# Kernel optimization log

Measured on AMD Instinct MI355X. Metric: run time of the kernel, lower is better.

The kernel has to match this reference:

```python
import jax, jax.numpy as jnp
import numpy as np

N_NODES = 100000
N_EDGES = 3200000
IN_CH = 256
OUT_CH = 10


def setup_inputs() -> dict:
    key = jax.random.key(0)
    k1, k2, k3, k4 = jax.random.split(key, 4)
    x = jax.random.normal(k1, (N_NODES, IN_CH), dtype=jnp.float32)
    edge_index = jax.random.randint(k2, (2, N_EDGES), 0, N_NODES, dtype=jnp.int64)
    W_mu = jax.random.normal(k3, (IN_CH, OUT_CH), dtype=jnp.float32) * (1.0 / np.sqrt(IN_CH))
    b_mu = jnp.zeros((OUT_CH,), dtype=jnp.float32)
    W_logstd = jax.random.normal(k4, (IN_CH, OUT_CH), dtype=jnp.float32) * (1.0 / np.sqrt(IN_CH))
    b_logstd = jnp.zeros((OUT_CH,), dtype=jnp.float32)
    return {"x": x, "edge_index": edge_index, "W_mu": W_mu, "b_mu": b_mu,
            "W_logstd": W_logstd, "b_logstd": b_logstd}


def _gcn_norm(edge_index, num_nodes):
    # PyG gcn_norm: add self loops, deg from target (col), norm = d^-1/2[row]*d^-1/2[col]
    loop = jnp.arange(num_nodes, dtype=edge_index.dtype)
    row = jnp.concatenate([edge_index[0], loop])  # source nodes
    col = jnp.concatenate([edge_index[1], loop])  # target nodes
    deg = jax.ops.segment_sum(jnp.ones_like(col, dtype=jnp.float32), col,
                              num_segments=num_nodes)
    dinv = jax.lax.rsqrt(jnp.maximum(deg, 1.0))  # self loops guarantee deg>=1
    norm = dinv[row] * dinv[col]  # [E+N]
    return row, col, norm


def _gcn_conv(x, W, b, row, col, norm, num_nodes):
    h = x @ W                               # [N, out]  linear transform first
    msg = h[row] * norm[:, None]            # gather + scale, [E+N, out]
    out = jax.ops.segment_sum(msg, col, num_segments=num_nodes)  # scatter-add
    return out + b


def reference(x, edge_index, W_mu, b_mu, W_logstd, b_logstd):
    n = x.shape[0]
    row, col, norm = _gcn_norm(edge_index, n)
    mu = _gcn_conv(x, W_mu, b_mu, row, col, norm, n)
    logstd = _gcn_conv(x, W_logstd, b_logstd, row, col, norm, n)
    return mu, logstd
```

## Files before the change

### kernel.cpp

```cpp
#include <hip/hip_runtime.h>
#include <math.h>

#define N_NODES 100000
#define N_EDGES 3200000
#define IN_CH 256
#define NC 20
#define OC 10
#define NPB 128
#define NBUCK 782
#define CAP 4864

#define CHUNK3 8192
#define NCHUNK3 391

__global__ __launch_bounds__(256) void k_initptr(int* __restrict__ bptr) {
    int i = blockIdx.x * 256 + threadIdx.x;
    if (i < NBUCK) bptr[i] = i * CAP;
}

__global__ __launch_bounds__(1024) void k_bin3(const int* __restrict__ row,
                                               const int* __restrict__ col,
                                               int* __restrict__ bptr,
                                               int* __restrict__ bpairs) {
    __shared__ int   lh[NBUCK];
    __shared__ int   lscan[NBUCK];
    __shared__ int   gmino[NBUCK];
    __shared__ int   stage[CHUNK3];
    __shared__ unsigned short sbkt[CHUNK3];

    int t = threadIdx.x;
    int e0 = blockIdx.x * CHUNK3;
    int nE = N_EDGES - e0; if (nE > CHUNK3) nE = CHUNK3;
    int n4 = nE >> 2;
    const int4* c4 = (const int4*)(col + e0);
    const int4* r4 = (const int4*)(row + e0);

    for (int i = t; i < NBUCK; i += 1024) lh[i] = 0;
    __syncthreads();

    for (int j = t; j < n4; j += 1024) {
        int4 c = c4[j];
        atomicAdd(&lh[c.x >> 7], 1); atomicAdd(&lh[c.y >> 7], 1);
        atomicAdd(&lh[c.z >> 7], 1); atomicAdd(&lh[c.w >> 7], 1);
    }
    __syncthreads();

    int cnt = 0;
    if (t < NBUCK) { cnt = lh[t]; lscan[t] = cnt; }
    __syncthreads();
    for (int o = 1; o < NBUCK; o <<= 1) {
        int add = 0;
        if (t < NBUCK && t >= o) add = lscan[t - o];
        __syncthreads();
        if (t < NBUCK) lscan[t] += add;
        __syncthreads();
    }
    if (t < NBUCK) {
        int lofs = lscan[t] - cnt;
        int gbase = cnt ? atomicAdd(&bptr[t], cnt) : 0;
        gmino[t] = gbase - lofs;
        lh[t] = lofs;
    }
    __syncthreads();

    for (int j = t; j < n4; j += 1024) {
        int4 c = c4[j];
        int4 r = r4[j];
        int b0 = c.x >> 7, b1 = c.y >> 7, b2 = c.z >> 7, b3 = c.w >> 7;
        int s0 = atomicAdd(&lh[b0], 1);
        int s1 = atomicAdd(&lh[b1], 1);
        int s2 = atomicAdd(&lh[b2], 1);
        int s3 = atomicAdd(&lh[b3], 1);
        stage[s0] = (r.x << 7) | (c.x & 127); sbkt[s0] = (unsigned short)b0;
        stage[s1] = (r.y << 7) | (c.y & 127); sbkt[s1] = (unsigned short)b1;
        stage[s2] = (r.z << 7) | (c.z & 127); sbkt[s2] = (unsigned short)b2;
        stage[s3] = (r.w << 7) | (c.w & 127); sbkt[s3] = (unsigned short)b3;
    }
    __syncthreads();

    for (int j = t; j < nE; j += 1024) {
        int b = sbkt[j];
        int dst = gmino[b] + j;
        if (dst < (b + 1) * CAP) bpairs[dst] = stage[j];
    }
}

__global__ __launch_bounds__(256) void k_deg(const int* __restrict__ bptr,
                                             const int* __restrict__ bpairs,
                                             float* __restrict__ dinv) {
    __shared__ int lc[NPB];
    int b = blockIdx.x, t = threadIdx.x;
    if (t < NPB) lc[t] = 0;
    __syncthreads();
    int start = b * CAP;
    int n = bptr[b] - start; if (n > CAP) n = CAP;
    for (int p = t; p < n; p += 256)
        atomicAdd(&lc[bpairs[start + p] & 127], 1);
    __syncthreads();
    int node = b * NPB + t;
    if (t < NPB && node < N_NODES)
        dinv[node] = rsqrtf((float)(lc[t] + 1));
}

__device__ __forceinline__ unsigned bfpack(float a, float b) {
    unsigned ua = __float_as_uint(a), ub = __float_as_uint(b);
    ua = (ua + 0x7FFFu + ((ua >> 16) & 1u)) >> 16;
    ub = (ub + 0x7FFFu + ((ub >> 16) & 1u)) >> 16;
    return ua | (ub << 16);
}
__device__ __forceinline__ float bflo(unsigned p) { return __uint_as_float(p << 16); }
__device__ __forceinline__ float bfhi(unsigned p) { return __uint_as_float(p & 0xFFFF0000u); }

__global__ __launch_bounds__(256) void k_gemm6(const float* __restrict__ x,
                                               const float* __restrict__ Wmu,
                                               const float* __restrict__ Wls,
                                               const float* __restrict__ dinv,
                                               unsigned* __restrict__ hbf) {
    __shared__ float sW[NC * 272];
    int t = threadIdx.x;
    for (int idx = t; idx < IN_CH * OC; idx += 256) {
        int k = idx / OC, c = idx - (idx / OC) * OC;
        int kk = k >> 6, j = k & 63;
        sW[c * 272 + kk * 68 + j]          = Wmu[idx];
        sW[(c + OC) * 272 + kk * 68 + j]   = Wls[idx];
    }
    __syncthreads();

    int kk = t & 3;
    int slot = t >> 2;
    int n0 = blockIdx.x * 128 + slot;

    int nd[2];
#pragma unroll
    for (int u = 0; u < 2; u++) {
        int n = n0 + u * 64;
        nd[u] = (n < N_NODES) ? n : (N_NODES - 1);
    }

    float acc[2][NC];
#pragma unroll
    for (int u = 0; u < 2; u++)
#pragma unroll
        for (int c = 0; c < NC; c++) acc[u][c] = 0.0f;

    const float4* x4 = (const float4*)x;

#pragma unroll 4
    for (int j4 = 0; j4 < 16; j4++) {
        float4 xv0 = x4[(size_t)nd[0] * 64 + kk * 16 + j4];
        float4 xv1 = x4[(size_t)nd[1] * 64 + kk * 16 + j4];
#pragma unroll
        for (int c = 0; c < NC; c++) {
            float4 w = *(const float4*)&sW[c * 272 + kk * 68 + j4 * 4];
            acc[0][c] += xv0.x * w.x + xv0.y * w.y + xv0.z * w.z + xv0.w * w.w;
            acc[1][c] += xv1.x * w.x + xv1.y * w.y + xv1.z * w.z + xv1.w * w.w;
        }
    }

#pragma unroll
    for (int u = 0; u < 2; u++)
#pragma unroll
        for (int c = 0; c < NC; c++) {
            acc[u][c] += __shfl_xor(acc[u][c], 2);
            acc[u][c] += __shfl_xor(acc[u][c], 1);
        }

    if (kk == 0) {
#pragma unroll
        for (int u = 0; u < 2; u++) {
            int n = n0 + u * 64;
            if (n >= N_NODES) continue;
            float d = dinv[n];
            unsigned* hp = hbf + (size_t)n * 10;
            *(uint2*)(hp + 0) = make_uint2(bfpack(acc[u][0] * d,  acc[u][1] * d),
                                           bfpack(acc[u][2] * d,  acc[u][3] * d));
            *(uint2*)(hp + 2) = make_uint2(bfpack(acc[u][4] * d,  acc[u][5] * d),
                                           bfpack(acc[u][6] * d,  acc[u][7] * d));
            *(uint2*)(hp + 4) = make_uint2(bfpack(acc[u][8] * d,  acc[u][9] * d),
                                           bfpack(acc[u][10] * d, acc[u][11] * d));
            *(uint2*)(hp + 6) = make_uint2(bfpack(acc[u][12] * d, acc[u][13] * d),
                                           bfpack(acc[u][14] * d, acc[u][15] * d));
            *(uint2*)(hp + 8) = make_uint2(bfpack(acc[u][16] * d, acc[u][17] * d),
                                           bfpack(acc[u][18] * d, acc[u][19] * d));
        }
    }
}

__global__ __launch_bounds__(256) void k_agg4(const int* __restrict__ bptr,
                                              const int* __restrict__ bpairs,
                                              const unsigned* __restrict__ hbf,
                                              const float* __restrict__ bmu,
                                              const float* __restrict__ bls,
                                              float* __restrict__ out) {
    __shared__ int lcnt[NPB];
    __shared__ int lscan[NPB];
    __shared__ int sCnt[NPB];
    __shared__ int ssrc[CAP];
    int b = blockIdx.x, t = threadIdx.x;
    int start = b * CAP;
    int n = bptr[b] - start; if (n > CAP) n = CAP;

    if (t < NPB) lcnt[t] = 0;
    __syncthreads();
    for (int p = t; p < n; p += 256)
        atomicAdd(&lcnt[bpairs[start + p] & 127], 1);
    __syncthreads();

    int cnt = 0;
    if (t < NPB) { cnt = lcnt[t]; lscan[t] = cnt; sCnt[t] = cnt; }
    __syncthreads();
    for (int o = 1; o < NPB; o <<= 1) {
        int add = 0;
        if (t < NPB && t >= o) add = lscan[t - o];
        __syncthreads();
        if (t < NPB) lscan[t] += add;
        __syncthreads();
    }
    if (t < NPB) lcnt[t] = lscan[t] - cnt;
    __syncthreads();

    for (int p = t; p < n; p += 256) {
        int pk = bpairs[start + p];
        int q = atomicAdd(&lcnt[pk & 127], 1);
        ssrc[q] = ((unsigned)pk) >> 7;
    }
    __syncthreads();

    int nl = t >> 1, half = t & 1;
    int node = b * NPB + nl;
    int ccnt = sCnt[nl];
    int base = lscan[nl] - ccnt;
    int mid = ccnt >> 1;
    int j0 = half ? mid : 0;
    int j1 = half ? ccnt : mid;

    float a[NC];
#pragma unroll
    for (int c = 0; c < NC; c++) a[c] = 0.0f;

#define ADDROW(R)                                                        \
    {                                                                    \
        const unsigned* hp_ = hbf + (size_t)(R) * 10;                    \
        uint2 q0 = *(const uint2*)(hp_ + 0);                             \
        uint2 q1 = *(const uint2*)(hp_ + 2);                             \
        uint2 q2 = *(const uint2*)(hp_ + 4);                             \
        uint2 q3 = *(const uint2*)(hp_ + 6);                             \
        uint2 q4 = *(const uint2*)(hp_ + 8);                             \
        a[0]  += bflo(q0.x); a[1]  += bfhi(q0.x);                        \
        a[2]  += bflo(q0.y); a[3]  += bfhi(q0.y);                        \
        a[4]  += bflo(q1.x); a[5]  += bfhi(q1.x);                        \
        a[6]  += bflo(q1.y); a[7]  += bfhi(q1.y);                        \
        a[8]  += bflo(q2.x); a[9]  += bfhi(q2.x);                        \
        a[10] += bflo(q2.y); a[11] += bfhi(q2.y);                        \
        a[12] += bflo(q3.x); a[13] += bfhi(q3.x);                        \
        a[14] += bflo(q3.y); a[15] += bfhi(q3.y);                        \
        a[16] += bflo(q4.x); a[17] += bfhi(q4.x);                        \
        a[18] += bflo(q4.y); a[19] += bfhi(q4.y);                        \
    }

    int j = j0;
    for (; j + 1 < j1; j += 2) {
        int r0 = ssrc[base + j];
        int r1 = ssrc[base + j + 1];
        ADDROW(r0);
        ADDROW(r1);
    }
    if (j < j1) {
        int r0 = ssrc[base + j];
        ADDROW(r0);
    }
    if (half == 0 && node < N_NODES) ADDROW(node);
#undef ADDROW

#pragma unroll
    for (int c = 0; c < NC; c++) a[c] += __shfl_xor(a[c], 1);

    if (half == 0 && node < N_NODES) {
        float dn = rsqrtf((float)(ccnt + 1));
        float* om = out + (size_t)node * OC;
        float* ol = out + (size_t)N_NODES * OC + (size_t)node * OC;
#pragma unroll
        for (int c = 0; c < OC; c++) {
            om[c] = dn * a[c]      + bmu[c];
            ol[c] = dn * a[c + OC] + bls[c];
        }
    }
}

__global__ __launch_bounds__(256) void k_init_deg(float* __restrict__ deg) {
    int i = blockIdx.x * 256 + threadIdx.x;
    if (i < N_NODES) deg[i] = 1.0f;
}
__global__ __launch_bounds__(256) void k_count(const int* __restrict__ col, float* __restrict__ deg) {
    int e = blockIdx.x * 256 + threadIdx.x;
    if (e < N_EDGES) atomicAdd(&deg[col[e]], 1.0f);
}
__global__ __launch_bounds__(256) void k_dinvk(float* __restrict__ deg) {
    int i = blockIdx.x * 256 + threadIdx.x;
    if (i < N_NODES) deg[i] = rsqrtf(deg[i]);
}
__global__ __launch_bounds__(256) void k_gemm_f32(const float* __restrict__ x,
                                                  const float* __restrict__ Wmu,
                                                  const float* __restrict__ Wls,
                                                  float* __restrict__ h) {
    int node = blockIdx.x * 256 + threadIdx.x;
    if (node >= N_NODES) return;
    const float4* x4 = (const float4*)(x + (size_t)node * IN_CH);
    float acc[NC];
#pragma unroll
    for (int c = 0; c < NC; c++) acc[c] = 0.0f;
    for (int k4 = 0; k4 < IN_CH / 4; k4++) {
        float4 xv = x4[k4];
        float xk[4] = {xv.x, xv.y, xv.z, xv.w};
#pragma unroll
        for (int kk = 0; kk < 4; kk++) {
            const float* wm = Wmu + (k4 * 4 + kk) * OC;
            const float* wl = Wls + (k4 * 4 + kk) * OC;
#pragma unroll
            for (int c = 0; c < OC; c++) {
                acc[c]      += xk[kk] * wm[c];
                acc[c + OC] += xk[kk] * wl[c];
            }
        }
    }
    float* hp = h + (size_t)node * NC;
#pragma unroll
    for (int c = 0; c < NC; c++) hp[c] = acc[c];
}
__global__ __launch_bounds__(256) void k_scatter(const int* __restrict__ row, const int* __restrict__ col,
                                                 const float* __restrict__ dinv, const float* __restrict__ h,
                                                 float* __restrict__ out) {
    int e = blockIdx.x * 256 + threadIdx.x;
    if (e >= N_EDGES) return;
    int r = row[e], c = col[e];
    float s = dinv[r] * dinv[c];
    const float* hp = h + (size_t)r * NC;
    float* om = out + (size_t)c * OC;
    float* ol = om + (size_t)N_NODES * OC;
#pragma unroll
    for (int k = 0; k < OC; k++) atomicAdd(om + k, hp[k] * s);
#pragma unroll
    for (int k = 0; k < OC; k++) atomicAdd(ol + k, hp[OC + k] * s);
}
__global__ __launch_bounds__(256) void k_final(const float* __restrict__ h, const float* __restrict__ dinv,
                                               const float* __restrict__ bmu, const float* __restrict__ bls,
                                               float* __restrict__ out) {
    int i = blockIdx.x * 256 + threadIdx.x;
    if (i >= N_NODES * OC) return;
    int node = i / OC, c = i - node * OC;
    float d = dinv[node];
    float d2 = d * d;
    out[i]                += h[node * NC + c]      * d2 + bmu[c];
    out[N_NODES * OC + i] += h[node * NC + OC + c] * d2 + bls[c];
}

extern "C" void kernel_launch(void* const* d_in, const int* in_sizes, int n_in,
                              void* d_out, int out_size, void* d_ws, size_t ws_size,
                              hipStream_t stream) {
    const float* x   = (const float*)d_in[0];
    const int*   ei  = (const int*)d_in[1];
    const float* Wmu = (const float*)d_in[2];
    const float* bmu = (const float*)d_in[3];
    const float* Wls = (const float*)d_in[4];
    const float* bls = (const float*)d_in[5];
    float* out = (float*)d_out;

    const int* row = ei;
    const int* col = ei + N_EDGES;

    const size_t BPAIRS_OFF = (size_t)(9 << 19);
    const size_t REQ = BPAIRS_OFF + (size_t)NBUCK * CAP * 4;

    if (ws_size >= REQ) {
        char* w = (char*)d_ws;
        int*      bptr   = (int*)(w);
        float*    dinv   = (float*)(w + 8192);
        unsigned* hbf    = (unsigned*)(w + (512 << 10));
        int*      bpairs = (int*)(w + BPAIRS_OFF);

        k_initptr<<<(NBUCK + 255) / 256, 256, 0, stream>>>(bptr);
        k_bin3<<<NCHUNK3, 1024, 0, stream>>>(row, col, bptr, bpairs);
        k_deg<<<NBUCK, 256, 0, stream>>>(bptr, bpairs, dinv);
        k_gemm6<<<(N_NODES + 127) / 128, 256, 0, stream>>>(x, Wmu, Wls, dinv, hbf);
        k_agg4<<<NBUCK, 256, 0, stream>>>(bptr, bpairs, hbf, bmu, bls, out);
    } else {
        float* deg = (float*)d_ws;
        float* h   = (float*)((char*)d_ws + (1 << 20));
        hipMemsetAsync(d_out, 0, (size_t)out_size * sizeof(float), stream);
        k_init_deg<<<(N_NODES + 255) / 256, 256, 0, stream>>>(deg);
        k_count<<<(N_EDGES + 255) / 256, 256, 0, stream>>>(col, deg);
        k_dinvk<<<(N_NODES + 255) / 256, 256, 0, stream>>>(deg);
        k_gemm_f32<<<(N_NODES + 255) / 256, 256, 0, stream>>>(x, Wmu, Wls, h);
        k_scatter<<<(N_EDGES + 255) / 256, 256, 0, stream>>>(row, col, deg, h, out);
        k_final<<<(N_NODES * OC + 255) / 256, 256, 0, stream>>>(h, deg, bmu, bls, out);
    }
}
```

Baseline: 262.1 us.

## Fuse degree counting into binning and cache bucket pairs in registers

Removes the separate degree kernel. In-degrees are now counted with global atomics inside the binning kernel, and the GEMM computes rsqrt from the integer degree. The aggregation kernel loads its bucket's pairs into registers once instead of reading them twice, and its gather loop is unrolled by four. This drops one launch and a pass over bpairs, but adds 3.2M scattered global atomics and raises register pressure in the aggregation kernel.

Result: slower. 381.1 us (+45.4%).

```diff
diff --git a/kernel.cpp b/kernel.cpp
--- a/kernel.cpp
+++ b/kernel.cpp
@@ -13,14 +13,17 @@
 #define CHUNK3 8192
 #define NCHUNK3 391
 
-__global__ __launch_bounds__(256) void k_initptr(int* __restrict__ bptr) {
+__global__ __launch_bounds__(256) void k_initptr2(int* __restrict__ bptr,
+                                                  int* __restrict__ deg) {
     int i = blockIdx.x * 256 + threadIdx.x;
     if (i < NBUCK) bptr[i] = i * CAP;
-}
-
-__global__ __launch_bounds__(1024) void k_bin3(const int* __restrict__ row,
+    if (i < N_NODES) deg[i] = 0;
+}
+
+__global__ __launch_bounds__(1024) void k_bin4(const int* __restrict__ row,
                                                const int* __restrict__ col,
                                                int* __restrict__ bptr,
+                                               int* __restrict__ deg,
                                                int* __restrict__ bpairs) {
     __shared__ int   lh[NBUCK];
     __shared__ int   lscan[NBUCK];
@@ -42,6 +45,8 @@
         int4 c = c4[j];
         atomicAdd(&lh[c.x >> 7], 1); atomicAdd(&lh[c.y >> 7], 1);
         atomicAdd(&lh[c.z >> 7], 1); atomicAdd(&lh[c.w >> 7], 1);
+        atomicAdd(&deg[c.x], 1); atomicAdd(&deg[c.y], 1);
+        atomicAdd(&deg[c.z], 1); atomicAdd(&deg[c.w], 1);
     }
     __syncthreads();
 
@@ -85,23 +90,6 @@
     }
 }
 
-__global__ __launch_bounds__(256) void k_deg(const int* __restrict__ bptr,
-                                             const int* __restrict__ bpairs,
-                                             float* __restrict__ dinv) {
-    __shared__ int lc[NPB];
-    int b = blockIdx.x, t = threadIdx.x;
-    if (t < NPB) lc[t] = 0;
-    __syncthreads();
-    int start = b * CAP;
-    int n = bptr[b] - start; if (n > CAP) n = CAP;
-    for (int p = t; p < n; p += 256)
-        atomicAdd(&lc[bpairs[start + p] & 127], 1);
-    __syncthreads();
-    int node = b * NPB + t;
-    if (t < NPB && node < N_NODES)
-        dinv[node] = rsqrtf((float)(lc[t] + 1));
-}
-
 __device__ __forceinline__ unsigned bfpack(float a, float b) {
     unsigned ua = __float_as_uint(a), ub = __float_as_uint(b);
     ua = (ua + 0x7FFFu + ((ua >> 16) & 1u)) >> 16;
@@ -111,11 +99,11 @@
 __device__ __forceinline__ float bflo(unsigned p) { return __uint_as_float(p << 16); }
 __device__ __forceinline__ float bfhi(unsigned p) { return __uint_as_float(p & 0xFFFF0000u); }
 
-__global__ __launch_bounds__(256) void k_gemm6(const float* __restrict__ x,
-                                               const float* __restrict__ Wmu,
-                                               const float* __restrict__ Wls,
-                                               const float* __restrict__ dinv,
-                                               unsigned* __restrict__ hbf) {
+__global__ __launch_bounds__(256) void k_gemm6b(const float* __restrict__ x,
+                                                const float* __restrict__ Wmu,
+                                                const float* __restrict__ Wls,
+                                                const int* __restrict__ deg,
+                                                unsigned* __restrict__ hbf) {
     __shared__ float sW[NC * 272];
     int t = threadIdx.x;
     for (int idx = t; idx < IN_CH * OC; idx += 256) {
@@ -170,7 +158,7 @@
         for (int u = 0; u < 2; u++) {
             int n = n0 + u * 64;
             if (n >= N_NODES) continue;
-            float d = dinv[n];
+            float d = rsqrtf((float)(deg[n] + 1));
             unsigned* hp = hbf + (size_t)n * 10;
             *(uint2*)(hp + 0) = make_uint2(bfpack(acc[u][0] * d,  acc[u][1] * d),
                                            bfpack(acc[u][2] * d,  acc[u][3] * d));
@@ -186,7 +174,7 @@
     }
 }
 
-__global__ __launch_bounds__(256) void k_agg4(const int* __restrict__ bptr,
+__global__ __launch_bounds__(256) void k_agg5(const int* __restrict__ bptr,
                                               const int* __restrict__ bpairs,
                                               const unsigned* __restrict__ hbf,
                                               const float* __restrict__ bmu,
@@ -200,10 +188,18 @@
     int start = b * CAP;
     int n = bptr[b] - start; if (n > CAP) n = CAP;
 
+    int myp[19];
+#pragma unroll
+    for (int i = 0; i < 19; i++) {
+        int p = t + i * 256;
+        myp[i] = (p < n) ? bpairs[start + p] : -1;
+    }
+
     if (t < NPB) lcnt[t] = 0;
     __syncthreads();
-    for (int p = t; p < n; p += 256)
-        atomicAdd(&lcnt[bpairs[start + p] & 127], 1);
+#pragma unroll
+    for (int i = 0; i < 19; i++)
+        if (myp[i] >= 0) atomicAdd(&lcnt[myp[i] & 127], 1);
     __syncthreads();
 
     int cnt = 0;
@@ -219,11 +215,12 @@
     if (t < NPB) lcnt[t] = lscan[t] - cnt;
     __syncthreads();
 
-    for (int p = t; p < n; p += 256) {
-        int pk = bpairs[start + p];
-        int q = atomicAdd(&lcnt[pk & 127], 1);
-        ssrc[q] = ((unsigned)pk) >> 7;
-    }
+#pragma unroll
+    for (int i = 0; i < 19; i++)
+        if (myp[i] >= 0) {
+            int q = atomicAdd(&lcnt[myp[i] & 127], 1);
+            ssrc[q] = ((unsigned)myp[i]) >> 7;
+        }
     __syncthreads();
 
     int nl = t >> 1, half = t & 1;
@@ -259,13 +256,17 @@
     }
 
     int j = j0;
-    for (; j + 1 < j1; j += 2) {
+    for (; j + 3 < j1; j += 4) {
         int r0 = ssrc[base + j];
         int r1 = ssrc[base + j + 1];
+        int r2 = ssrc[base + j + 2];
+        int r3 = ssrc[base + j + 3];
         ADDROW(r0);
         ADDROW(r1);
-    }
-    if (j < j1) {
+        ADDROW(r2);
+        ADDROW(r3);
+    }
+    for (; j < j1; j++) {
         int r0 = ssrc[base + j];
         ADDROW(r0);
     }
@@ -374,15 +375,14 @@
     if (ws_size >= REQ) {
         char* w = (char*)d_ws;
         int*      bptr   = (int*)(w);
-        float*    dinv   = (float*)(w + 8192);
+        int*      deg    = (int*)(w + 8192);
         unsigned* hbf    = (unsigned*)(w + (512 << 10));
         int*      bpairs = (int*)(w + BPAIRS_OFF);
 
-        k_initptr<<<(NBUCK + 255) / 256, 256, 0, stream>>>(bptr);
-        k_bin3<<<NCHUNK3, 1024, 0, stream>>>(row, col, bptr, bpairs);
-        k_deg<<<NBUCK, 256, 0, stream>>>(bptr, bpairs, dinv);
-        k_gemm6<<<(N_NODES + 127) / 128, 256, 0, stream>>>(x, Wmu, Wls, dinv, hbf);
-        k_agg4<<<NBUCK, 256, 0, stream>>>(bptr, bpairs, hbf, bmu, bls, out);
+        k_initptr2<<<(N_NODES + 255) / 256, 256, 0, stream>>>(bptr, deg);
+        k_bin4<<<NCHUNK3, 1024, 0, stream>>>(row, col, bptr, deg, bpairs);
+        k_gemm6b<<<(N_NODES + 127) / 128, 256, 0, stream>>>(x, Wmu, Wls, deg, hbf);
+        k_agg5<<<NBUCK, 256, 0, stream>>>(bptr, bpairs, hbf, bmu, bls, out);
     } else {
         float* deg = (float*)d_ws;
         float* h   = (float*)((char*)d_ws + (1 << 20));
```
